# Optimization experiments

Hardware: AMD Instinct MI355X
Metric: run time of the kernel (lower is better)

The kernel has to match this reference:

```python
import jax, jax.numpy as jnp
import numpy as np

NUM_SEGMENTS = 8192  # number of graphs in the batch (max(batch)+1 in the torch code)
EPS = 1e-10


def setup_inputs() -> dict:
    key = jax.random.key(0)
    k1, k2 = jax.random.split(key)
    N, D = 2_000_000, 32
    batch = jnp.sort(jax.random.randint(k1, (N,), 0, NUM_SEGMENTS, dtype=jnp.int64))
    x = jax.random.normal(k2, (N, D), dtype=jnp.float32)
    return {"batch": batch, "input": x}


def reference(batch, input):
    # segment-wise numerically-stable softmax over nodes sharing a batch id
    # seg_max: [S, D]; empty segments get -inf but are never gathered
    seg_max = jax.ops.segment_max(input, batch, num_segments=NUM_SEGMENTS)
    x = jnp.exp(input - seg_max[batch])            # [N, D]
    norm = jax.ops.segment_sum(x, batch, num_segments=NUM_SEGMENTS)[batch]  # [N, D]
    return x / (norm + EPS)
```

## Files before the change

kernel.cpp:

```cpp
#include <hip/hip_runtime.h>
#include <math.h>

#define NSEG 8192
#define D 32
#define EPSF 1e-10f
#define ROWS_CAP 512
#define BLK 256

__global__ void init_starts_kernel(int* __restrict__ seg_start, int N) {
    int s = blockIdx.x * blockDim.x + threadIdx.x;
    if (s <= NSEG) seg_start[s] = N;
}

__global__ void find_starts_kernel(const int* __restrict__ batch,
                                   int* __restrict__ seg_start, int N) {
    int i = blockIdx.x * blockDim.x + threadIdx.x;
    if (i >= N) return;
    int b = batch[i];
    int prev = (i == 0) ? -1 : batch[i - 1];
    for (int s = prev + 1; s <= b; ++s) seg_start[s] = i;
}

__device__ __forceinline__ float4 f4max(float4 a, float4 b) {
    return make_float4(fmaxf(a.x, b.x), fmaxf(a.y, b.y),
                       fmaxf(a.z, b.z), fmaxf(a.w, b.w));
}
__device__ __forceinline__ float4 f4add(float4 a, float4 b) {
    return make_float4(a.x + b.x, a.y + b.y, a.z + b.z, a.w + b.w);
}
__device__ __forceinline__ float4 shfl_xor_f4(float4 v, int mask) {
    return make_float4(__shfl_xor(v.x, mask, 64), __shfl_xor(v.y, mask, 64),
                       __shfl_xor(v.z, mask, 64), __shfl_xor(v.w, mask, 64));
}

__global__ __launch_bounds__(BLK, 2) void seg_softmax_kernel(
    const float* __restrict__ x, const int* __restrict__ seg_start,
    float* __restrict__ out)
{
    __shared__ float4 xbuf[ROWS_CAP * (D / 4)];
    __shared__ float4 red[4 * (D / 4)];

    const int s     = blockIdx.x;
    const int start = seg_start[s];
    const int end   = seg_start[s + 1];
    const int len   = end - start;
    if (len <= 0) return;

    const int tid  = (int)threadIdx.x;
    const int cg   = tid & 7;
    const int rg   = tid >> 3;
    const int wave = tid >> 6;
    const int lane = tid & 63;

    const float4* __restrict__ xin  = (const float4*)(x   + (size_t)start * D);
    float4* __restrict__       outv = (float4*)      (out + (size_t)start * D);

    const float4 neg_inf4 = make_float4(-INFINITY, -INFINITY, -INFINITY, -INFINITY);

    if (len <= ROWS_CAP) {
        float4 lmax = neg_inf4;
        for (int r = rg; r < len; r += 32) {
            float4 v = xin[r * 8 + cg];
            xbuf[r * 8 + cg] = v;
            lmax = f4max(lmax, v);
        }
        lmax = f4max(lmax, shfl_xor_f4(lmax, 8));
        lmax = f4max(lmax, shfl_xor_f4(lmax, 16));
        lmax = f4max(lmax, shfl_xor_f4(lmax, 32));
        if (lane < 8) red[wave * 8 + cg] = lmax;
        __syncthreads();
        float4 cmax = f4max(f4max(red[0 * 8 + cg], red[1 * 8 + cg]),
                            f4max(red[2 * 8 + cg], red[3 * 8 + cg]));
        __syncthreads();

        float4 lsum = make_float4(0.f, 0.f, 0.f, 0.f);
        for (int r = rg; r < len; r += 32) {
            float4 v = xbuf[r * 8 + cg];
            float4 e;
            e.x = __expf(v.x - cmax.x);
            e.y = __expf(v.y - cmax.y);
            e.z = __expf(v.z - cmax.z);
            e.w = __expf(v.w - cmax.w);
            xbuf[r * 8 + cg] = e;
            lsum = f4add(lsum, e);
        }
        lsum = f4add(lsum, shfl_xor_f4(lsum, 8));
        lsum = f4add(lsum, shfl_xor_f4(lsum, 16));
        lsum = f4add(lsum, shfl_xor_f4(lsum, 32));
        if (lane < 8) red[wave * 8 + cg] = lsum;
        __syncthreads();
        float4 csum = f4add(f4add(red[0 * 8 + cg], red[1 * 8 + cg]),
                            f4add(red[2 * 8 + cg], red[3 * 8 + cg]));
        float4 rnorm = make_float4(1.f / (csum.x + EPSF), 1.f / (csum.y + EPSF),
                                   1.f / (csum.z + EPSF), 1.f / (csum.w + EPSF));

        for (int r = rg; r < len; r += 32) {
            float4 e = xbuf[r * 8 + cg];
            e.x *= rnorm.x; e.y *= rnorm.y; e.z *= rnorm.z; e.w *= rnorm.w;
            outv[r * 8 + cg] = e;
        }
    } else {
        float4 lmax = neg_inf4;
        for (int r = rg; r < len; r += 32)
            lmax = f4max(lmax, xin[r * 8 + cg]);
        lmax = f4max(lmax, shfl_xor_f4(lmax, 8));
        lmax = f4max(lmax, shfl_xor_f4(lmax, 16));
        lmax = f4max(lmax, shfl_xor_f4(lmax, 32));
        if (lane < 8) red[wave * 8 + cg] = lmax;
        __syncthreads();
        float4 cmax = f4max(f4max(red[0 * 8 + cg], red[1 * 8 + cg]),
                            f4max(red[2 * 8 + cg], red[3 * 8 + cg]));
        __syncthreads();

        float4 lsum = make_float4(0.f, 0.f, 0.f, 0.f);
        for (int r = rg; r < len; r += 32) {
            float4 v = xin[r * 8 + cg];
            float4 e;
            e.x = __expf(v.x - cmax.x);
            e.y = __expf(v.y - cmax.y);
            e.z = __expf(v.z - cmax.z);
            e.w = __expf(v.w - cmax.w);
            outv[r * 8 + cg] = e;
            lsum = f4add(lsum, e);
        }
        lsum = f4add(lsum, shfl_xor_f4(lsum, 8));
        lsum = f4add(lsum, shfl_xor_f4(lsum, 16));
        lsum = f4add(lsum, shfl_xor_f4(lsum, 32));
        if (lane < 8) red[wave * 8 + cg] = lsum;
        __syncthreads();
        float4 csum = f4add(f4add(red[0 * 8 + cg], red[1 * 8 + cg]),
                            f4add(red[2 * 8 + cg], red[3 * 8 + cg]));
        float4 rnorm = make_float4(1.f / (csum.x + EPSF), 1.f / (csum.y + EPSF),
                                   1.f / (csum.z + EPSF), 1.f / (csum.w + EPSF));

        for (int r = rg; r < len; r += 32) {
            float4 e = outv[r * 8 + cg];
            e.x *= rnorm.x; e.y *= rnorm.y; e.z *= rnorm.z; e.w *= rnorm.w;
            outv[r * 8 + cg] = e;
        }
    }
}

extern "C" void kernel_launch(void* const* d_in, const int* in_sizes, int n_in,
                              void* d_out, int out_size, void* d_ws, size_t ws_size,
                              hipStream_t stream) {
    const int*   batch = (const int*)d_in[0];
    const float* x     = (const float*)d_in[1];
    float*       out   = (float*)d_out;
    const int    N     = in_sizes[0];

    int* seg_start = (int*)d_ws;

    init_starts_kernel<<<(NSEG + 1 + 255) / 256, 256, 0, stream>>>(seg_start, N);
    find_starts_kernel<<<(N + 255) / 256, 256, 0, stream>>>(batch, seg_start, N);
    seg_softmax_kernel<<<NSEG, BLK, 0, stream>>>(x, seg_start, out);
}
```

Measured before the change: 466.0 us.

## Use one wave per segment with online softmax and nontemporal stores

Replaces the block-per-segment kernel, which staged rows in shared memory, with one 64-lane wave per segment. Each wave computes max and sum in a single online-softmax pass, merges partial results through shuffles without LDS or __syncthreads, then re-reads the input and writes normalized outputs with nontemporal stores. Global traffic becomes two reads and one write per element. The online update adds extra exponentials per element, and each segment (about 244 rows) now has only a single wave of parallelism.

```diff
diff --git a/kernel.cpp b/kernel.cpp
--- a/kernel.cpp
+++ b/kernel.cpp
@@ -4,8 +4,8 @@
 #define NSEG 8192
 #define D 32
 #define EPSF 1e-10f
-#define ROWS_CAP 512
 #define BLK 256
+#define WPB 4
 
 __global__ void init_starts_kernel(int* __restrict__ seg_start, int N) {
     int s = blockIdx.x * blockDim.x + threadIdx.x;
@@ -21,123 +21,79 @@
     for (int s = prev + 1; s <= b; ++s) seg_start[s] = i;
 }
 
-__device__ __forceinline__ float4 f4max(float4 a, float4 b) {
-    return make_float4(fmaxf(a.x, b.x), fmaxf(a.y, b.y),
-                       fmaxf(a.z, b.z), fmaxf(a.w, b.w));
-}
-__device__ __forceinline__ float4 f4add(float4 a, float4 b) {
-    return make_float4(a.x + b.x, a.y + b.y, a.z + b.z, a.w + b.w);
-}
-__device__ __forceinline__ float4 shfl_xor_f4(float4 v, int mask) {
-    return make_float4(__shfl_xor(v.x, mask, 64), __shfl_xor(v.y, mask, 64),
-                       __shfl_xor(v.z, mask, 64), __shfl_xor(v.w, mask, 64));
+typedef float v4f __attribute__((ext_vector_type(4)));
+
+__device__ __forceinline__ v4f shfl_xor_v4(v4f v, int mask) {
+    v4f r;
+    r.x = __shfl_xor(v.x, mask, 64);
+    r.y = __shfl_xor(v.y, mask, 64);
+    r.z = __shfl_xor(v.z, mask, 64);
+    r.w = __shfl_xor(v.w, mask, 64);
+    return r;
 }
 
-__global__ __launch_bounds__(BLK, 2) void seg_softmax_kernel(
+#define ONLINE_ACC(c)                                          \
+    {                                                          \
+        float mn = fmaxf(m.c, v.c);                            \
+        l.c = l.c * __expf(m.c - mn) + __expf(v.c - mn);       \
+        m.c = mn;                                              \
+    }
+
+#define ONLINE_MERGE(c)                                        \
+    {                                                          \
+        float mn = fmaxf(m.c, m2.c);                           \
+        l.c = l.c * __expf(m.c - mn) + l2.c * __expf(m2.c - mn); \
+        m.c = mn;                                              \
+    }
+
+__global__ __launch_bounds__(BLK, 8) void seg_softmax_wave(
     const float* __restrict__ x, const int* __restrict__ seg_start,
     float* __restrict__ out)
 {
-    __shared__ float4 xbuf[ROWS_CAP * (D / 4)];
-    __shared__ float4 red[4 * (D / 4)];
+    const int tid  = (int)threadIdx.x;
+    const int lane = tid & 63;
+    const int s    = blockIdx.x * WPB + (tid >> 6);
 
-    const int s     = blockIdx.x;
     const int start = seg_start[s];
-    const int end   = seg_start[s + 1];
-    const int len   = end - start;
+    const int len   = seg_start[s + 1] - start;
     if (len <= 0) return;
 
-    const int tid  = (int)threadIdx.x;
-    const int cg   = tid & 7;
-    const int rg   = tid >> 3;
-    const int wave = tid >> 6;
-    const int lane = tid & 63;
+    const int cg = lane & 7;
+    const int rg = lane >> 3;
 
-    const float4* __restrict__ xin  = (const float4*)(x   + (size_t)start * D);
-    float4* __restrict__       outv = (float4*)      (out + (size_t)start * D);
+    const v4f* __restrict__ xin = (const v4f*)(x + (size_t)start * D);
+    v4f* __restrict__       outv = (v4f*)(out + (size_t)start * D);
 
-    const float4 neg_inf4 = make_float4(-INFINITY, -INFINITY, -INFINITY, -INFINITY);
+    const float LOW = -1e30f;
+    v4f m = {LOW, LOW, LOW, LOW};
+    v4f l = {0.f, 0.f, 0.f, 0.f};
 
-    if (len <= ROWS_CAP) {
-        float4 lmax = neg_inf4;
-        for (int r = rg; r < len; r += 32) {
-            float4 v = xin[r * 8 + cg];
-            xbuf[r * 8 + cg] = v;
-            lmax = f4max(lmax, v);
-        }
-        lmax = f4max(lmax, shfl_xor_f4(lmax, 8));
-        lmax = f4max(lmax, shfl_xor_f4(lmax, 16));
-        lmax = f4max(lmax, shfl_xor_f4(lmax, 32));
-        if (lane < 8) red[wave * 8 + cg] = lmax;
-        __syncthreads();
-        float4 cmax = f4max(f4max(red[0 * 8 + cg], red[1 * 8 + cg]),
-                            f4max(red[2 * 8 + cg], red[3 * 8 + cg]));
-        __syncthreads();
+    for (int r = rg; r < len; r += 8) {
+        v4f v = xin[r * 8 + cg];
+        ONLINE_ACC(x) ONLINE_ACC(y) ONLINE_ACC(z) ONLINE_ACC(w)
+    }
 
-        float4 lsum = make_float4(0.f, 0.f, 0.f, 0.f);
-        for (int r = rg; r < len; r += 32) {
-            float4 v = xbuf[r * 8 + cg];
-            float4 e;
-            e.x = __expf(v.x - cmax.x);
-            e.y = __expf(v.y - cmax.y);
-            e.z = __expf(v.z - cmax.z);
-            e.w = __expf(v.w - cmax.w);
-            xbuf[r * 8 + cg] = e;
-            lsum = f4add(lsum, e);
-        }
-        lsum = f4add(lsum, shfl_xor_f4(lsum, 8));
-        lsum = f4add(lsum, shfl_xor_f4(lsum, 16));
-        lsum = f4add(lsum, shfl_xor_f4(lsum, 32));
-        if (lane < 8) red[wave * 8 + cg] = lsum;
-        __syncthreads();
-        float4 csum = f4add(f4add(red[0 * 8 + cg], red[1 * 8 + cg]),
-                            f4add(red[2 * 8 + cg], red[3 * 8 + cg]));
-        float4 rnorm = make_float4(1.f / (csum.x + EPSF), 1.f / (csum.y + EPSF),
-                                   1.f / (csum.z + EPSF), 1.f / (csum.w + EPSF));
+    #pragma unroll
+    for (int mask = 8; mask <= 32; mask <<= 1) {
+        v4f m2 = shfl_xor_v4(m, mask);
+        v4f l2 = shfl_xor_v4(l, mask);
+        ONLINE_MERGE(x) ONLINE_MERGE(y) ONLINE_MERGE(z) ONLINE_MERGE(w)
+    }
 
-        for (int r = rg; r < len; r += 32) {
-            float4 e = xbuf[r * 8 + cg];
-            e.x *= rnorm.x; e.y *= rnorm.y; e.z *= rnorm.z; e.w *= rnorm.w;
-            outv[r * 8 + cg] = e;
-        }
-    } else {
-        float4 lmax = neg_inf4;
-        for (int r = rg; r < len; r += 32)
-            lmax = f4max(lmax, xin[r * 8 + cg]);
-        lmax = f4max(lmax, shfl_xor_f4(lmax, 8));
-        lmax = f4max(lmax, shfl_xor_f4(lmax, 16));
-        lmax = f4max(lmax, shfl_xor_f4(lmax, 32));
-        if (lane < 8) red[wave * 8 + cg] = lmax;
-        __syncthreads();
-        float4 cmax = f4max(f4max(red[0 * 8 + cg], red[1 * 8 + cg]),
-                            f4max(red[2 * 8 + cg], red[3 * 8 + cg]));
-        __syncthreads();
+    v4f rn;
+    rn.x = 1.f / (l.x + EPSF);
+    rn.y = 1.f / (l.y + EPSF);
+    rn.z = 1.f / (l.z + EPSF);
+    rn.w = 1.f / (l.w + EPSF);
 
-        float4 lsum = make_float4(0.f, 0.f, 0.f, 0.f);
-        for (int r = rg; r < len; r += 32) {
-            float4 v = xin[r * 8 + cg];
-            float4 e;
-            e.x = __expf(v.x - cmax.x);
-            e.y = __expf(v.y - cmax.y);
-            e.z = __expf(v.z - cmax.z);
-            e.w = __expf(v.w - cmax.w);
-            outv[r * 8 + cg] = e;
-            lsum = f4add(lsum, e);
-        }
-        lsum = f4add(lsum, shfl_xor_f4(lsum, 8));
-        lsum = f4add(lsum, shfl_xor_f4(lsum, 16));
-        lsum = f4add(lsum, shfl_xor_f4(lsum, 32));
-        if (lane < 8) red[wave * 8 + cg] = lsum;
-        __syncthreads();
-        float4 csum = f4add(f4add(red[0 * 8 + cg], red[1 * 8 + cg]),
-                            f4add(red[2 * 8 + cg], red[3 * 8 + cg]));
-        float4 rnorm = make_float4(1.f / (csum.x + EPSF), 1.f / (csum.y + EPSF),
-                                   1.f / (csum.z + EPSF), 1.f / (csum.w + EPSF));
-
-        for (int r = rg; r < len; r += 32) {
-            float4 e = outv[r * 8 + cg];
-            e.x *= rnorm.x; e.y *= rnorm.y; e.z *= rnorm.z; e.w *= rnorm.w;
-            outv[r * 8 + cg] = e;
-        }
+    for (int r = rg; r < len; r += 8) {
+        v4f v = xin[r * 8 + cg];
+        v4f e;
+        e.x = __expf(v.x - m.x) * rn.x;
+        e.y = __expf(v.y - m.y) * rn.y;
+        e.z = __expf(v.z - m.z) * rn.z;
+        e.w = __expf(v.w - m.w) * rn.w;
+        __builtin_nontemporal_store(e, &outv[r * 8 + cg]);
     }
 }
 
@@ -153,5 +109,5 @@
 
     init_starts_kernel<<<(NSEG + 1 + 255) / 256, 256, 0, stream>>>(seg_start, N);
     find_starts_kernel<<<(N + 255) / 256, 256, 0, stream>>>(batch, seg_start, N);
-    seg_softmax_kernel<<<NSEG, BLK, 0, stream>>>(x, seg_start, out);
+    seg_softmax_wave<<<NSEG / WPB, BLK, 0, stream>>>(x, seg_start, out);
 }
```

Measured after the change: 470.5 us. Within noise of the previous version (+1.0%).
